# Optimization experiments

Hardware: AMD Instinct MI355X
Metric: run time of the kernel (lower is better)

## Reference

```python
import jax, jax.numpy as jnp
import numpy as np

VOCAB, EMB, HID = 32000, 128, 256
B, T = 512, 512


def setup_inputs() -> dict:
    key = jax.random.key(0)
    ks = jax.random.split(key, 6)
    x = jax.random.randint(ks[0], (B, T), 0, VOCAB, dtype=jnp.int64) if jax.config.jax_enable_x64 else jax.random.randint(ks[0], (B, T), 0, VOCAB, dtype=jnp.int32)
    s_e = 1.0 / np.sqrt(HID)
    emb = jax.random.normal(ks[1], (VOCAB, EMB), dtype=jnp.float32)
    W_ih = jax.random.uniform(ks[2], (3 * HID, EMB), dtype=jnp.float32, minval=-s_e, maxval=s_e)
    W_hh = jax.random.uniform(ks[3], (3 * HID, HID), dtype=jnp.float32, minval=-s_e, maxval=s_e)
    b_ih = jax.random.uniform(ks[4], (3 * HID,), dtype=jnp.float32, minval=-s_e, maxval=s_e)
    b_hh = jax.random.uniform(ks[5], (3 * HID,), dtype=jnp.float32, minval=-s_e, maxval=s_e)
    return {"x": x, "emb": emb, "W_ih": W_ih, "W_hh": W_hh, "b_ih": b_ih, "b_hh": b_hh}


def reference(x, emb, W_ih, W_hh, b_ih, b_hh):
    # in_len = x.shape[0] per original code (loops x[:, t, :] for t in range(x.shape[0]))
    in_len = x.shape[0]
    H = W_hh.shape[1]
    xe = emb[x]                                   # [B, T, E]
    xs = jnp.swapaxes(xe[:, :in_len, :], 0, 1)    # [in_len, B, E]
    # precompute input-side gate projections for all timesteps (one big GEMM)
    gi = jnp.einsum('tbe,ge->tbg', xs, W_ih) + b_ih   # [in_len, B, 3H]

    def step(h, gi_t):
        gh = h @ W_hh.T + b_hh                    # [B, 3H]
        i_r, i_z, i_n = gi_t[:, :H], gi_t[:, H:2*H], gi_t[:, 2*H:]
        h_r, h_z, h_n = gh[:, :H], gh[:, H:2*H], gh[:, 2*H:]
        r = jax.nn.sigmoid(i_r + h_r)
        z = jax.nn.sigmoid(i_z + h_z)
        n = jnp.tanh(i_n + r * h_n)
        h_new = (1.0 - z) * n + z * h
        return h_new, None

    h0 = jnp.zeros((x.shape[0], H), dtype=emb.dtype)  # batch = x.shape[0]
    hT, _ = jax.lax.scan(step, h0, gi)
    return hT
```

## Files before the change

kernel.cpp:

```cpp
#include <hip/hip_runtime.h>


typedef unsigned short ushort_t;
typedef __attribute__((ext_vector_type(8))) short short8;
typedef __attribute__((ext_vector_type(4))) float float4_;
typedef __attribute__((ext_vector_type(4))) unsigned short ushort4_;

#define VOCAB 32000
#define EMB 128
#define HID 256
#define G3 768
#define BB 512
#define TT 512
#define SLOT 786432
#define BLK_BYTES 24576
#define WFIXED 8781824

__device__ __forceinline__ float b2f(ushort_t u) {
  return __uint_as_float(((unsigned)u) << 16);
}
__device__ __forceinline__ ushort_t f2b(float f) {
  unsigned u = __float_as_uint(f);
  return (ushort_t)((u + 0x7FFFu + ((u >> 16) & 1u)) >> 16);
}
__device__ __forceinline__ short8 ld8(const ushort_t* p) { return *(const short8*)p; }
__device__ __forceinline__ void gld_lds16(const void* g, void* l) {
  __builtin_amdgcn_global_load_lds((const __attribute__((address_space(1))) void*)g,
                                   (__attribute__((address_space(3))) void*)l, 16, 0, 0);
}
__device__ __forceinline__ int gi_byte(int bl, int twog) {
  return ((bl * 1536) + twog) ^ ((bl & 7) << 4);
}

__global__ void cvt_bf16_k(const float* __restrict__ s, ushort_t* __restrict__ d, int n4) {
  int i = blockIdx.x * blockDim.x + threadIdx.x;
  int stride = gridDim.x * blockDim.x;
  for (; i < n4; i += stride) {
    float4_ v = ((const float4_*)s)[i];
    ushort4_ o;
    o.x = f2b(v.x); o.y = f2b(v.y); o.z = f2b(v.z); o.w = f2b(v.w);
    ((ushort4_*)d)[i] = o;
  }
}

__global__ __launch_bounds__(256) void gi_gemm(
    const int* __restrict__ x, const ushort_t* __restrict__ emb16,
    const ushort_t* __restrict__ Wih16, const float* __restrict__ bih,
    const float* __restrict__ bhh, char* __restrict__ gic, int t0) {
  __shared__ float cb[G3];
  const int tid = threadIdx.x;
  for (int i = tid; i < G3; i += 256) cb[i] = bih[i] + (i < 512 ? bhh[i] : 0.f);
  __syncthreads();
  const int lane = tid & 63, w = tid >> 6;
  const int bl = lane & 15, kg = lane >> 4;
  const int nt0 = (blockIdx.x * 4 + w) * 4;

  short8 bfr[4][4];
#pragma unroll
  for (int j = 0; j < 4; ++j) {
    int nt = nt0 + j;
    int b = (nt & 31) * 16 + bl;
    int tok = x[b * TT + t0 + (nt >> 5)];
#pragma unroll
    for (int kt = 0; kt < 4; ++kt)
      bfr[j][kt] = ld8(emb16 + (size_t)tok * EMB + kt * 32 + kg * 8);
  }

#pragma unroll 1
  for (int mt = 0; mt < 48; ++mt) {
    short8 af[4];
#pragma unroll
    for (int kt = 0; kt < 4; ++kt)
      af[kt] = ld8(Wih16 + (mt * 16 + bl) * EMB + kt * 32 + kg * 8);
    float4_ z4 = {0.f, 0.f, 0.f, 0.f};
    float4_ acc[4] = {z4, z4, z4, z4};
#pragma unroll
    for (int kt = 0; kt < 4; ++kt) {
#pragma unroll
      for (int j = 0; j < 4; ++j)
        acc[j] = __builtin_amdgcn_mfma_f32_16x16x32_bf16(af[kt], bfr[j][kt], acc[j], 0, 0, 0);
    }
    int byte8 = gi_byte(bl, 32 * mt + 8 * kg);
#pragma unroll
    for (int j = 0; j < 4; ++j) {
      int nt = nt0 + j;
      size_t base = (size_t)(nt >> 5) * SLOT + (size_t)(nt & 31) * BLK_BYTES;
      ushort4_ o;
#pragma unroll
      for (int r = 0; r < 4; ++r)
        o[r] = f2b(acc[j][r] + cb[mt * 16 + kg * 4 + r]);
      *(ushort4_*)(gic + base + byte8) = o;
    }
  }
}

__global__ __launch_bounds__(512, 2) void gru_rec(
    const ushort_t* __restrict__ Whh16, const char* __restrict__ gic,
    const float* __restrict__ bhh, float* __restrict__ out, int t0, int C) {
  __shared__ alignas(16) ushort_t h_lds[2][16 * HID];
  __shared__ alignas(16) char gi_lds[2][BLK_BYTES];
  __shared__ float bhn_lds[HID];

  const int tid = threadIdx.x, lane = tid & 63, w = tid >> 6;
  const int bl = lane & 15, kg = lane >> 4;
  const int b0 = blockIdx.x * 16;
  const char* gblk = gic + (size_t)blockIdx.x * BLK_BYTES;

  if (t0 == 0) {
    for (int i = tid; i < 16 * HID; i += 512) h_lds[0][i] = 0;
  } else {
    for (int i = tid; i < 16 * HID; i += 512) {
      int b = i >> 8, k = i & 255;
      *(ushort_t*)((char*)h_lds[0] + (((b << 9) + 2 * k) ^ ((b & 7) << 4))) =
          f2b(out[(size_t)(b0 + b) * HID + k]);
    }
  }
  for (int i = tid; i < HID; i += 512) bhn_lds[i] = bhh[512 + i];

  short8 wf[2][3][8];
#pragma unroll
  for (int i = 0; i < 2; ++i) {
#pragma unroll
    for (int q = 0; q < 3; ++q) {
      int g = (w + 8 * i + 16 * q) * 16 + bl;
#pragma unroll
      for (int kt = 0; kt < 8; ++kt)
        wf[i][q][kt] = ld8(Whh16 + (size_t)g * HID + kt * 32 + kg * 8);
    }
  }

  float hreg[2][4];
#pragma unroll
  for (int i = 0; i < 2; ++i) {
    if (t0 == 0) {
#pragma unroll
      for (int r = 0; r < 4; ++r) hreg[i][r] = 0.f;
    } else {
      float4_ v = *(const float4_*)&out[(size_t)(b0 + bl) * HID + (w + 8 * i) * 16 + kg * 4];
#pragma unroll
      for (int r = 0; r < 4; ++r) hreg[i][r] = v[r];
    }
  }

  {
    int o = (w * 3) * 1024;
#pragma unroll
    for (int ii = 0; ii < 3; ++ii)
      gld_lds16(gblk + o + ii * 1024 + lane * 16, &gi_lds[0][o + ii * 1024]);
  }
  __syncthreads();

#pragma unroll 1
  for (int t = 0; t < C; ++t) {
    const int cur = t & 1, nxt = cur ^ 1;
    if (t + 1 < C) {
      const char* src = gblk + (size_t)(t + 1) * SLOT + (w * 3) * 1024;
#pragma unroll
      for (int ii = 0; ii < 3; ++ii)
        gld_lds16(src + ii * 1024 + lane * 16, &gi_lds[nxt][(w * 3) * 1024 + ii * 1024]);
    }

    float4_ acc[2][3];
#pragma unroll
    for (int i = 0; i < 2; ++i) {
#pragma unroll
      for (int q = 0; q < 2; ++q) {
        int byte8 = gi_byte(bl, 32 * (w + 8 * i + 16 * q) + 8 * kg);
        ushort4_ v = *(const ushort4_*)(&gi_lds[cur][byte8]);
#pragma unroll
        for (int r = 0; r < 4; ++r) acc[i][q][r] = b2f(v[r]);
      }
      acc[i][2] = *(const float4_*)&bhn_lds[(w + 8 * i) * 16 + kg * 4];
    }

#pragma unroll
    for (int kt = 0; kt < 8; ++kt) {
      int byteoff = ((bl * 512) + (kt * 32 + kg * 8) * 2) ^ ((bl & 7) << 4);
      short8 bf = *(const short8*)((const char*)h_lds[cur] + byteoff);
#pragma unroll
      for (int i = 0; i < 2; ++i) {
#pragma unroll
        for (int q = 0; q < 3; ++q)
          acc[i][q] = __builtin_amdgcn_mfma_f32_16x16x32_bf16(wf[i][q][kt], bf, acc[i][q], 0, 0, 0);
      }
    }

#pragma unroll
    for (int i = 0; i < 2; ++i) {
      int byte8n = gi_byte(bl, 32 * (32 + w + 8 * i) + 8 * kg);
      ushort4_ gv = *(const ushort4_*)(&gi_lds[cur][byte8n]);
#pragma unroll
      for (int r = 0; r < 4; ++r) {
        float xr = acc[i][0][r];
        float xz = acc[i][1][r];
        float hn = acc[i][2][r];
        float rr = __builtin_amdgcn_rcpf(1.f + __expf(-xr));
        float zz = __builtin_amdgcn_rcpf(1.f + __expf(-xz));
        float y = b2f(gv[r]) + rr * hn;
        float nn = 1.f - 2.f * __builtin_amdgcn_rcpf(1.f + __expf(2.f * y));
        hreg[i][r] = (1.f - zz) * nn + zz * hreg[i][r];
      }
      int j0 = (w + 8 * i) * 16 + kg * 4;
      unsigned lo = (unsigned)f2b(hreg[i][0]) | ((unsigned)f2b(hreg[i][1]) << 16);
      unsigned hi = (unsigned)f2b(hreg[i][2]) | ((unsigned)f2b(hreg[i][3]) << 16);
      int byte0 = (bl * 512 + j0 * 2) ^ ((bl & 7) << 4);
      char* hp = (char*)h_lds[nxt];
      *(unsigned*)(hp + byte0) = lo;
      *(unsigned*)(hp + byte0 + 4) = hi;
    }
    __syncthreads();
  }

#pragma unroll
  for (int i = 0; i < 2; ++i) {
    float4_ v = {hreg[i][0], hreg[i][1], hreg[i][2], hreg[i][3]};
    *(float4_*)&out[(size_t)(b0 + bl) * HID + (w + 8 * i) * 16 + kg * 4] = v;
  }
}

extern "C" void kernel_launch(void* const* d_in, const int* in_sizes, int n_in,
                              void* d_out, int out_size, void* d_ws, size_t ws_size,
                              hipStream_t stream) {
  const int* x = (const int*)d_in[0];
  const float* emb = (const float*)d_in[1];
  const float* Wih = (const float*)d_in[2];
  const float* Whh = (const float*)d_in[3];
  const float* bih = (const float*)d_in[4];
  const float* bhh = (const float*)d_in[5];
  float* out = (float*)d_out;

  char* ws = (char*)d_ws;
  ushort_t* emb16 = (ushort_t*)ws;
  ushort_t* Wih16 = (ushort_t*)(ws + 8192000);
  ushort_t* Whh16 = (ushort_t*)(ws + 8388608);
  char* gic = ws + WFIXED;

  size_t avail = ws_size > (size_t)WFIXED ? ws_size - (size_t)WFIXED : 0;
  int C = (int)(avail / (size_t)SLOT);
  if (C > TT) C = TT;
  if (C < 1) C = 1;

  cvt_bf16_k<<<1024, 256, 0, stream>>>(emb, emb16, (VOCAB * EMB) / 4);
  cvt_bf16_k<<<96, 256, 0, stream>>>(Wih, Wih16, (G3 * EMB) / 4);
  cvt_bf16_k<<<192, 256, 0, stream>>>(Whh, Whh16, (G3 * HID) / 4);

  for (int t0 = 0; t0 < TT; t0 += C) {
    int Cc = TT - t0 < C ? TT - t0 : C;
    gi_gemm<<<2 * Cc, 256, 0, stream>>>(x, emb16, Wih16, bih, bhh, gic, t0);
    gru_rec<<<32, 512, 0, stream>>>(Whh16, gic, bhh, out, t0, Cc);
  }
}
```

Before: 1.439 ms.

## Deepen gi prefetch ring in GRU recurrence and stage gi_gemm output through LDS

The recurrent kernel now uses a 4-slot LDS ring with a prefetch distance of three steps and explicit vmcnt waits plus raw s_barrier instead of __syncthreads. The aim is to hide global-load latency for the per-step input gate projections on the serial critical path. gi_gemm is reorganised so each block handles one batch tile for two timesteps, splitting gate rows across waves and staging results in LDS for coalesced 16-byte stores. The b_hn bias moves from LDS into registers. The hand-managed waitcnt counts are fragile if the compiler emits extra vector memory ops, and the larger LDS ring may limit occupancy.

```diff
diff --git a/kernel.cpp b/kernel.cpp
--- a/kernel.cpp
+++ b/kernel.cpp
@@ -5,6 +5,7 @@
 typedef __attribute__((ext_vector_type(8))) short short8;
 typedef __attribute__((ext_vector_type(4))) float float4_;
 typedef __attribute__((ext_vector_type(4))) unsigned short ushort4_;
+typedef __attribute__((ext_vector_type(2))) unsigned int uint2_;
 
 #define VOCAB 32000
 #define EMB 128
@@ -46,50 +47,60 @@
 __global__ __launch_bounds__(256) void gi_gemm(
     const int* __restrict__ x, const ushort_t* __restrict__ emb16,
     const ushort_t* __restrict__ Wih16, const float* __restrict__ bih,
-    const float* __restrict__ bhh, char* __restrict__ gic, int t0) {
+    const float* __restrict__ bhh, char* __restrict__ gic, int t0, int C) {
   __shared__ float cb[G3];
+  __shared__ alignas(16) char img[2][BLK_BYTES];
   const int tid = threadIdx.x;
   for (int i = tid; i < G3; i += 256) cb[i] = bih[i] + (i < 512 ? bhh[i] : 0.f);
-  __syncthreads();
   const int lane = tid & 63, w = tid >> 6;
   const int bl = lane & 15, kg = lane >> 4;
-  const int nt0 = (blockIdx.x * 4 + w) * 4;
-
-  short8 bfr[4][4];
-#pragma unroll
-  for (int j = 0; j < 4; ++j) {
-    int nt = nt0 + j;
-    int b = (nt & 31) * 16 + bl;
-    int tok = x[b * TT + t0 + (nt >> 5)];
+  const int blk = blockIdx.x & 31;
+  const int tt0 = (blockIdx.x >> 5) * 2;
+  const int nj = (C - tt0) < 2 ? 1 : 2;
+
+  short8 bfr[2][4];
+#pragma unroll
+  for (int j = 0; j < 2; ++j) {
+    int tloc = tt0 + (j < nj ? j : 0);
+    int tok = x[(blk * 16 + bl) * TT + t0 + tloc];
 #pragma unroll
     for (int kt = 0; kt < 4; ++kt)
       bfr[j][kt] = ld8(emb16 + (size_t)tok * EMB + kt * 32 + kg * 8);
   }
+  __syncthreads();
 
 #pragma unroll 1
-  for (int mt = 0; mt < 48; ++mt) {
+  for (int mi = 0; mi < 12; ++mi) {
+    int mt = w * 12 + mi;
     short8 af[4];
 #pragma unroll
     for (int kt = 0; kt < 4; ++kt)
       af[kt] = ld8(Wih16 + (mt * 16 + bl) * EMB + kt * 32 + kg * 8);
     float4_ z4 = {0.f, 0.f, 0.f, 0.f};
-    float4_ acc[4] = {z4, z4, z4, z4};
-#pragma unroll
-    for (int kt = 0; kt < 4; ++kt) {
-#pragma unroll
-      for (int j = 0; j < 4; ++j)
+    float4_ acc[2] = {z4, z4};
+#pragma unroll
+    for (int kt = 0; kt < 4; ++kt)
+#pragma unroll
+      for (int j = 0; j < 2; ++j)
         acc[j] = __builtin_amdgcn_mfma_f32_16x16x32_bf16(af[kt], bfr[j][kt], acc[j], 0, 0, 0);
-    }
     int byte8 = gi_byte(bl, 32 * mt + 8 * kg);
 #pragma unroll
-    for (int j = 0; j < 4; ++j) {
-      int nt = nt0 + j;
-      size_t base = (size_t)(nt >> 5) * SLOT + (size_t)(nt & 31) * BLK_BYTES;
+    for (int j = 0; j < 2; ++j) {
       ushort4_ o;
 #pragma unroll
-      for (int r = 0; r < 4; ++r)
-        o[r] = f2b(acc[j][r] + cb[mt * 16 + kg * 4 + r]);
-      *(ushort4_*)(gic + base + byte8) = o;
+      for (int r = 0; r < 4; ++r) o[r] = f2b(acc[j][r] + cb[mt * 16 + kg * 4 + r]);
+      *(ushort4_*)(&img[j][byte8]) = o;
+    }
+  }
+  __syncthreads();
+
+#pragma unroll
+  for (int j = 0; j < 2; ++j) {
+    if (j < nj) {
+      char* dst = gic + (size_t)(tt0 + j) * SLOT + (size_t)blk * BLK_BYTES;
+#pragma unroll
+      for (int c = 0; c < 6; ++c)
+        *(float4_*)(dst + c * 4096 + tid * 16) = *(const float4_*)(&img[j][c * 4096 + tid * 16]);
     }
   }
 }
@@ -98,8 +109,7 @@
     const ushort_t* __restrict__ Whh16, const char* __restrict__ gic,
     const float* __restrict__ bhh, float* __restrict__ out, int t0, int C) {
   __shared__ alignas(16) ushort_t h_lds[2][16 * HID];
-  __shared__ alignas(16) char gi_lds[2][BLK_BYTES];
-  __shared__ float bhn_lds[HID];
+  __shared__ alignas(16) char gi_ring[4][BLK_BYTES];
 
   const int tid = threadIdx.x, lane = tid & 63, w = tid >> 6;
   const int bl = lane & 15, kg = lane >> 4;
@@ -115,11 +125,10 @@
           f2b(out[(size_t)(b0 + b) * HID + k]);
     }
   }
-  for (int i = tid; i < HID; i += 512) bhn_lds[i] = bhh[512 + i];
 
   short8 wf[2][3][8];
 #pragma unroll
-  for (int i = 0; i < 2; ++i) {
+  for (int i = 0; i < 2; ++i)
 #pragma unroll
     for (int q = 0; q < 3; ++q) {
       int g = (w + 8 * i + 16 * q) * 16 + bl;
@@ -127,11 +136,12 @@
       for (int kt = 0; kt < 8; ++kt)
         wf[i][q][kt] = ld8(Whh16 + (size_t)g * HID + kt * 32 + kg * 8);
     }
-  }
-
+
+  float4_ bhn[2];
   float hreg[2][4];
 #pragma unroll
   for (int i = 0; i < 2; ++i) {
+    bhn[i] = *(const float4_*)&bhh[512 + (w + 8 * i) * 16 + kg * 4];
     if (t0 == 0) {
 #pragma unroll
       for (int r = 0; r < 4; ++r) hreg[i][r] = 0.f;
@@ -142,22 +152,38 @@
     }
   }
 
-  {
-    int o = (w * 3) * 1024;
-#pragma unroll
-    for (int ii = 0; ii < 3; ++ii)
-      gld_lds16(gblk + o + ii * 1024 + lane * 16, &gi_lds[0][o + ii * 1024]);
-  }
-  __syncthreads();
+  asm volatile("s_waitcnt vmcnt(0) lgkmcnt(0)" ::: "memory");
+  __builtin_amdgcn_s_barrier();
+  __builtin_amdgcn_sched_barrier(0);
+
+#pragma unroll
+  for (int tau = 0; tau < 3; ++tau) {
+    if (tau < C) {
+      const char* src = gblk + (size_t)tau * SLOT + (w * 3) * 1024 + lane * 16;
+      char* dst = &gi_ring[tau][(w * 3) * 1024];
+#pragma unroll
+      for (int ii = 0; ii < 3; ++ii) gld_lds16(src + ii * 1024, dst + ii * 1024);
+    }
+  }
 
 #pragma unroll 1
   for (int t = 0; t < C; ++t) {
-    const int cur = t & 1, nxt = cur ^ 1;
-    if (t + 1 < C) {
-      const char* src = gblk + (size_t)(t + 1) * SLOT + (w * 3) * 1024;
-#pragma unroll
-      for (int ii = 0; ii < 3; ++ii)
-        gld_lds16(src + ii * 1024 + lane * 16, &gi_lds[nxt][(w * 3) * 1024 + ii * 1024]);
+    int rem = C - 1 - t;
+    if (rem >= 2)
+      asm volatile("s_waitcnt vmcnt(6) lgkmcnt(0)" ::: "memory");
+    else if (rem == 1)
+      asm volatile("s_waitcnt vmcnt(3) lgkmcnt(0)" ::: "memory");
+    else
+      asm volatile("s_waitcnt vmcnt(0) lgkmcnt(0)" ::: "memory");
+    __builtin_amdgcn_s_barrier();
+    __builtin_amdgcn_sched_barrier(0);
+
+    const int slot = t & 3, cur = t & 1, nxt = cur ^ 1;
+    if (t + 3 < C) {
+      const char* src = gblk + (size_t)(t + 3) * SLOT + (w * 3) * 1024 + lane * 16;
+      char* dst = &gi_ring[(t + 3) & 3][(w * 3) * 1024];
+#pragma unroll
+      for (int ii = 0; ii < 3; ++ii) gld_lds16(src + ii * 1024, dst + ii * 1024);
     }
 
     float4_ acc[2][3];
@@ -166,49 +192,42 @@
 #pragma unroll
       for (int q = 0; q < 2; ++q) {
         int byte8 = gi_byte(bl, 32 * (w + 8 * i + 16 * q) + 8 * kg);
-        ushort4_ v = *(const ushort4_*)(&gi_lds[cur][byte8]);
+        ushort4_ v = *(const ushort4_*)(&gi_ring[slot][byte8]);
 #pragma unroll
         for (int r = 0; r < 4; ++r) acc[i][q][r] = b2f(v[r]);
       }
-      acc[i][2] = *(const float4_*)&bhn_lds[(w + 8 * i) * 16 + kg * 4];
+      acc[i][2] = bhn[i];
     }
 
 #pragma unroll
     for (int kt = 0; kt < 8; ++kt) {
-      int byteoff = ((bl * 512) + (kt * 32 + kg * 8) * 2) ^ ((bl & 7) << 4);
+      int byteoff = ((bl * 512) + kt * 64 + kg * 16) ^ ((bl & 7) << 4);
       short8 bf = *(const short8*)((const char*)h_lds[cur] + byteoff);
 #pragma unroll
-      for (int i = 0; i < 2; ++i) {
+      for (int i = 0; i < 2; ++i)
 #pragma unroll
         for (int q = 0; q < 3; ++q)
           acc[i][q] = __builtin_amdgcn_mfma_f32_16x16x32_bf16(wf[i][q][kt], bf, acc[i][q], 0, 0, 0);
-      }
     }
 
 #pragma unroll
     for (int i = 0; i < 2; ++i) {
       int byte8n = gi_byte(bl, 32 * (32 + w + 8 * i) + 8 * kg);
-      ushort4_ gv = *(const ushort4_*)(&gi_lds[cur][byte8n]);
+      ushort4_ gv = *(const ushort4_*)(&gi_ring[slot][byte8n]);
 #pragma unroll
       for (int r = 0; r < 4; ++r) {
-        float xr = acc[i][0][r];
-        float xz = acc[i][1][r];
-        float hn = acc[i][2][r];
-        float rr = __builtin_amdgcn_rcpf(1.f + __expf(-xr));
-        float zz = __builtin_amdgcn_rcpf(1.f + __expf(-xz));
-        float y = b2f(gv[r]) + rr * hn;
+        float rr = __builtin_amdgcn_rcpf(1.f + __expf(-acc[i][0][r]));
+        float zz = __builtin_amdgcn_rcpf(1.f + __expf(-acc[i][1][r]));
+        float y = b2f(gv[r]) + rr * acc[i][2][r];
         float nn = 1.f - 2.f * __builtin_amdgcn_rcpf(1.f + __expf(2.f * y));
         hreg[i][r] = (1.f - zz) * nn + zz * hreg[i][r];
       }
-      int j0 = (w + 8 * i) * 16 + kg * 4;
-      unsigned lo = (unsigned)f2b(hreg[i][0]) | ((unsigned)f2b(hreg[i][1]) << 16);
-      unsigned hi = (unsigned)f2b(hreg[i][2]) | ((unsigned)f2b(hreg[i][3]) << 16);
-      int byte0 = (bl * 512 + j0 * 2) ^ ((bl & 7) << 4);
-      char* hp = (char*)h_lds[nxt];
-      *(unsigned*)(hp + byte0) = lo;
-      *(unsigned*)(hp + byte0 + 4) = hi;
-    }
-    __syncthreads();
+      int byte0 = (bl * 512 + ((w + 8 * i) * 16 + kg * 4) * 2) ^ ((bl & 7) << 4);
+      uint2_ hv;
+      hv.x = (unsigned)f2b(hreg[i][0]) | ((unsigned)f2b(hreg[i][1]) << 16);
+      hv.y = (unsigned)f2b(hreg[i][2]) | ((unsigned)f2b(hreg[i][3]) << 16);
+      *(uint2_*)((char*)h_lds[nxt] + byte0) = hv;
+    }
   }
 
 #pragma unroll
@@ -246,7 +265,7 @@
 
   for (int t0 = 0; t0 < TT; t0 += C) {
     int Cc = TT - t0 < C ? TT - t0 : C;
-    gi_gemm<<<2 * Cc, 256, 0, stream>>>(x, emb16, Wih16, bih, bhh, gic, t0);
+    gi_gemm<<<((Cc + 1) / 2) * 32, 256, 0, stream>>>(x, emb16, Wih16, bih, bhh, gic, t0, Cc);
     gru_rec<<<32, 512, 0, stream>>>(Whh16, gic, bhh, out, t0, Cc);
   }
 }
```

After: 1.521 ms. 1.06x slower.

## Precompute per-vocab gate table and gather it inside a single recurrent kernel

Applied to the files above, without the earlier changes.

Instead of computing input gate projections for every (t,b) token, a table of W_ih·emb+bias is computed once per vocabulary entry (32000 rows), and the recurrent kernel gathers rows by token id via direct-to-LDS loads with a 4-deep prefetch ring. The log2(e) scaling is folded into W_hh, the table and the biases so the activations can use raw exp2 instead of expf. The chunked multi-launch loop is replaced by one persistent launch, and the step loop is unrolled by four with explicit waitcnt/barrier control. This removes the large B*T gate GEMM and its workspace traffic, but adds scattered gathers of table rows on the critical path.

```diff
diff --git a/kernel.cpp b/kernel.cpp
--- a/kernel.cpp
+++ b/kernel.cpp
@@ -5,20 +5,17 @@
 typedef __attribute__((ext_vector_type(8))) short short8;
 typedef __attribute__((ext_vector_type(4))) float float4_;
 typedef __attribute__((ext_vector_type(4))) unsigned short ushort4_;
+typedef __attribute__((ext_vector_type(2))) unsigned int uint2_;
+typedef __attribute__((ext_vector_type(4))) int int4_;
 
 #define VOCAB 32000
 #define EMB 128
 #define HID 256
 #define G3 768
-#define BB 512
 #define TT 512
-#define SLOT 786432
-#define BLK_BYTES 24576
-#define WFIXED 8781824
-
-__device__ __forceinline__ float b2f(ushort_t u) {
-  return __uint_as_float(((unsigned)u) << 16);
-}
+#define L2E 1.4426950408889634f
+#define L2E2 2.8853900817779268f
+
 __device__ __forceinline__ ushort_t f2b(float f) {
   unsigned u = __float_as_uint(f);
   return (ushort_t)((u + 0x7FFFu + ((u >> 16) & 1u)) >> 16);
@@ -28,8 +25,17 @@
   __builtin_amdgcn_global_load_lds((const __attribute__((address_space(1))) void*)g,
                                    (__attribute__((address_space(3))) void*)l, 16, 0, 0);
 }
-__device__ __forceinline__ int gi_byte(int bl, int twog) {
-  return ((bl * 1536) + twog) ^ ((bl & 7) << 4);
+__device__ __forceinline__ float exp2pos(float x) {
+#if __has_builtin(__builtin_amdgcn_exp2f)
+  return __builtin_amdgcn_exp2f(x);
+#else
+  float r; asm("v_exp_f32 %0, %1" : "=v"(r) : "v"(x)); return r;
+#endif
+}
+__device__ __forceinline__ float exp2neg(float x) { return exp2pos(-x); }
+__device__ __forceinline__ unsigned pkbf(float a, float b) {
+  unsigned r; asm("v_cvt_pk_bf16_f32 %0, %1, %2" : "=v"(r) : "v"(a), "v"(b));
+  return r;
 }
 
 __global__ void cvt_bf16_k(const float* __restrict__ s, ushort_t* __restrict__ d, int n4) {
@@ -42,84 +48,97 @@
     ((ushort4_*)d)[i] = o;
   }
 }
-
-__global__ __launch_bounds__(256) void gi_gemm(
-    const int* __restrict__ x, const ushort_t* __restrict__ emb16,
-    const ushort_t* __restrict__ Wih16, const float* __restrict__ bih,
-    const float* __restrict__ bhh, char* __restrict__ gic, int t0) {
-  __shared__ float cb[G3];
+__global__ void cvt_whh_k(const float* __restrict__ s, ushort_t* __restrict__ d) {
+  int i = blockIdx.x * blockDim.x + threadIdx.x;
+  if (i >= (G3 * HID) / 4) return;
+  float sc = ((i >> 6) < 512) ? L2E : L2E2;
+  float4_ v = ((const float4_*)s)[i];
+  ushort4_ o;
+  o.x = f2b(v.x * sc); o.y = f2b(v.y * sc); o.z = f2b(v.z * sc); o.w = f2b(v.w * sc);
+  ((ushort4_*)d)[i] = o;
+}
+
+__global__ __launch_bounds__(256) void tbl_gemm(
+    const ushort_t* __restrict__ emb16, const ushort_t* __restrict__ Wih16,
+    const float* __restrict__ bih, const float* __restrict__ bhh,
+    char* __restrict__ tb_out) {
+  __shared__ float cbs[G3];
+  __shared__ alignas(16) char img[16 * 1552];
   const int tid = threadIdx.x;
-  for (int i = tid; i < G3; i += 256) cb[i] = bih[i] + (i < 512 ? bhh[i] : 0.f);
-  __syncthreads();
+  for (int i = tid; i < G3; i += 256) {
+    float sc = (i < 512) ? L2E : L2E2;
+    cbs[i] = sc * (bih[i] + (i < 512 ? bhh[i] : 0.f));
+  }
   const int lane = tid & 63, w = tid >> 6;
   const int bl = lane & 15, kg = lane >> 4;
-  const int nt0 = (blockIdx.x * 4 + w) * 4;
-
-  short8 bfr[4][4];
-#pragma unroll
-  for (int j = 0; j < 4; ++j) {
-    int nt = nt0 + j;
-    int b = (nt & 31) * 16 + bl;
-    int tok = x[b * TT + t0 + (nt >> 5)];
-#pragma unroll
-    for (int kt = 0; kt < 4; ++kt)
-      bfr[j][kt] = ld8(emb16 + (size_t)tok * EMB + kt * 32 + kg * 8);
-  }
+  const int v0 = blockIdx.x * 16;
+
+  short8 bfr[4];
+#pragma unroll
+  for (int kt = 0; kt < 4; ++kt)
+    bfr[kt] = ld8(emb16 + (size_t)(v0 + bl) * EMB + kt * 32 + kg * 8);
+  __syncthreads();
 
 #pragma unroll 1
-  for (int mt = 0; mt < 48; ++mt) {
+  for (int mi = 0; mi < 12; ++mi) {
+    int mt = w * 12 + mi;
     short8 af[4];
 #pragma unroll
     for (int kt = 0; kt < 4; ++kt)
       af[kt] = ld8(Wih16 + (mt * 16 + bl) * EMB + kt * 32 + kg * 8);
-    float4_ z4 = {0.f, 0.f, 0.f, 0.f};
-    float4_ acc[4] = {z4, z4, z4, z4};
-#pragma unroll
-    for (int kt = 0; kt < 4; ++kt) {
-#pragma unroll
-      for (int j = 0; j < 4; ++j)
-        acc[j] = __builtin_amdgcn_mfma_f32_16x16x32_bf16(af[kt], bfr[j][kt], acc[j], 0, 0, 0);
-    }
-    int byte8 = gi_byte(bl, 32 * mt + 8 * kg);
-#pragma unroll
-    for (int j = 0; j < 4; ++j) {
-      int nt = nt0 + j;
-      size_t base = (size_t)(nt >> 5) * SLOT + (size_t)(nt & 31) * BLK_BYTES;
-      ushort4_ o;
-#pragma unroll
-      for (int r = 0; r < 4; ++r)
-        o[r] = f2b(acc[j][r] + cb[mt * 16 + kg * 4 + r]);
-      *(ushort4_*)(gic + base + byte8) = o;
-    }
-  }
-}
+    float4_ acc = {0.f, 0.f, 0.f, 0.f};
+#pragma unroll
+    for (int kt = 0; kt < 4; ++kt)
+      acc = __builtin_amdgcn_mfma_f32_16x16x32_bf16(af[kt], bfr[kt], acc, 0, 0, 0);
+    float sc = (mt < 32) ? L2E : L2E2;
+    int g0 = mt * 16 + kg * 4;
+    float v0f = fmaf(sc, acc[0], cbs[g0 + 0]);
+    float v1f = fmaf(sc, acc[1], cbs[g0 + 1]);
+    float v2f = fmaf(sc, acc[2], cbs[g0 + 2]);
+    float v3f = fmaf(sc, acc[3], cbs[g0 + 3]);
+    uint2_ o;
+    o.x = pkbf(v0f, v1f);
+    o.y = pkbf(v2f, v3f);
+    *(uint2_*)(img + bl * 1552 + mt * 32 + kg * 8) = o;
+  }
+  __syncthreads();
+
+#pragma unroll
+  for (int c = 0; c < 6; ++c) {
+    int p = c * 4096 + tid * 16;
+    int q = p >> 9;
+    int row = (q * 21846) >> 16;
+    int off = p - row * 1536;
+    float4_ v = *(const float4_*)(img + row * 1552 + off);
+    *(float4_*)(tb_out + (size_t)(v0 + row) * 1536 + off) = v;
+  }
+}
+
+#define WAITV(N) asm volatile("s_waitcnt vmcnt(" #N ") lgkmcnt(0)" ::: "memory")
 
 __global__ __launch_bounds__(512, 2) void gru_rec(
-    const ushort_t* __restrict__ Whh16, const char* __restrict__ gic,
-    const float* __restrict__ bhh, float* __restrict__ out, int t0, int C) {
-  __shared__ alignas(16) ushort_t h_lds[2][16 * HID];
-  __shared__ alignas(16) char gi_lds[2][BLK_BYTES];
-  __shared__ float bhn_lds[HID];
+    const ushort_t* __restrict__ Whh16, const char* __restrict__ tbl,
+    const float* __restrict__ bhh, const int* __restrict__ x,
+    float* __restrict__ out) {
+  __shared__ alignas(16) char smem[147456];
 
   const int tid = threadIdx.x, lane = tid & 63, w = tid >> 6;
   const int bl = lane & 15, kg = lane >> 4;
   const int b0 = blockIdx.x * 16;
-  const char* gblk = gic + (size_t)blockIdx.x * BLK_BYTES;
-
-  if (t0 == 0) {
-    for (int i = tid; i < 16 * HID; i += 512) h_lds[0][i] = 0;
-  } else {
-    for (int i = tid; i < 16 * HID; i += 512) {
-      int b = i >> 8, k = i & 255;
-      *(ushort_t*)((char*)h_lds[0] + (((b << 9) + 2 * k) ^ ((b & 7) << 4))) =
-          f2b(out[(size_t)(b0 + b) * HID + k]);
-    }
-  }
-  for (int i = tid; i < HID; i += 512) bhn_lds[i] = bhh[512 + i];
+  const int s16 = (bl & 7) << 4;
+
+  {
+    const int4_* xs = (const int4_*)(x + (size_t)b0 * TT);
+    int4_* xd = (int4_*)(smem + 114688);
+#pragma unroll
+    for (int i = 0; i < 4; ++i) xd[tid + i * 512] = xs[tid + i * 512];
+    int4_ z4 = {0, 0, 0, 0};
+    *(int4_*)(smem + 98304 + tid * 16) = z4;
+  }
 
   short8 wf[2][3][8];
 #pragma unroll
-  for (int i = 0; i < 2; ++i) {
+  for (int i = 0; i < 2; ++i)
 #pragma unroll
     for (int q = 0; q < 3; ++q) {
       int g = (w + 8 * i + 16 * q) * 16 + bl;
@@ -127,89 +146,127 @@
       for (int kt = 0; kt < 8; ++kt)
         wf[i][q][kt] = ld8(Whh16 + (size_t)g * HID + kt * 32 + kg * 8);
     }
-  }
-
+
+  int h_off[8], gi_off[2][2], gn_off[2], hw_off[2];
+#pragma unroll
+  for (int kt = 0; kt < 8; ++kt)
+    h_off[kt] = 98304 + ((bl * 512 + kt * 64 + kg * 16) ^ s16);
+#pragma unroll
+  for (int i = 0; i < 2; ++i) {
+#pragma unroll
+    for (int q = 0; q < 2; ++q)
+      gi_off[i][q] = (bl * 1536 + 32 * (w + 8 * i + 16 * q) + 8 * kg) ^ s16;
+    gn_off[i] = (bl * 1536 + 32 * (32 + w + 8 * i) + 8 * kg) ^ s16;
+    hw_off[i] = 98304 + ((bl * 512 + ((w + 8 * i) * 16 + kg * 4) * 2) ^ s16);
+  }
+
+  const int s0 = (2 * w) & 7, s1 = (2 * w + 1) & 7;
+  const unsigned inv0 = (unsigned)((lane * 16) ^ (s0 << 4));
+  const unsigned inv1 = (lane < 32) ? (unsigned)((1024 + lane * 16) ^ (s0 << 4))
+                                    : (unsigned)((lane * 16 - 512) ^ (s1 << 4));
+  const unsigned inv2 = (unsigned)((512 + lane * 16) ^ (s1 << 4));
+
+  float4_ bhn[2];
   float hreg[2][4];
 #pragma unroll
   for (int i = 0; i < 2; ++i) {
-    if (t0 == 0) {
-#pragma unroll
-      for (int r = 0; r < 4; ++r) hreg[i][r] = 0.f;
-    } else {
-      float4_ v = *(const float4_*)&out[(size_t)(b0 + bl) * HID + (w + 8 * i) * 16 + kg * 4];
-#pragma unroll
-      for (int r = 0; r < 4; ++r) hreg[i][r] = v[r];
-    }
-  }
-
+    float4_ bv = *(const float4_*)&bhh[512 + (w + 8 * i) * 16 + kg * 4];
+#pragma unroll
+    for (int r = 0; r < 4; ++r) { bhn[i][r] = L2E2 * bv[r]; hreg[i][r] = 0.f; }
+  }
+
+  const int* xp = (const int*)(smem + 114688) + 2 * w * 512;
+  __syncthreads();
+
+#pragma unroll
+  for (int tau = 0; tau < 3; ++tau) {
+    int tA = xp[tau];
+    int tB = xp[tau + 512];
+    unsigned aA = (unsigned)tA * 1536u;
+    unsigned aB = (unsigned)tB * 1536u;
+    unsigned aM = (lane < 32) ? aA : aB;
+    char* d0 = smem + tau * 24576 + w * 3072;
+    gld_lds16(tbl + aA + inv0, d0);
+    gld_lds16(tbl + aM + inv1, d0 + 1024);
+    gld_lds16(tbl + aB + inv2, d0 + 2048);
+  }
+
+#define STEP(K, SL, PAR, WN, DOPF) do { \
+    WAITV(WN); \
+    __builtin_amdgcn_s_barrier(); \
+    __builtin_amdgcn_sched_barrier(0); \
+    if (DOPF) { \
+      int tA = xp[xb + (K)]; \
+      int tB = xp[xb + (K) + 512]; \
+      unsigned aA = (unsigned)tA * 1536u; \
+      unsigned aB = (unsigned)tB * 1536u; \
+      unsigned aM = (lane < 32) ? aA : aB; \
+      char* d0 = smem + (((K) + 3) & 3) * 24576 + w * 3072; \
+      gld_lds16(tbl + aA + inv0, d0); \
+      gld_lds16(tbl + aM + inv1, d0 + 1024); \
+      gld_lds16(tbl + aB + inv2, d0 + 2048); \
+    } \
+    float4_ acc[2][3]; \
+    _Pragma("unroll") for (int i = 0; i < 2; ++i) { \
+      _Pragma("unroll") for (int q = 0; q < 2; ++q) { \
+        uint2_ dg = *(const uint2_*)(smem + (SL) * 24576 + gi_off[i][q]); \
+        acc[i][q][0] = __uint_as_float(dg.x << 16); \
+        acc[i][q][1] = __uint_as_float(dg.x & 0xFFFF0000u); \
+        acc[i][q][2] = __uint_as_float(dg.y << 16); \
+        acc[i][q][3] = __uint_as_float(dg.y & 0xFFFF0000u); \
+      } \
+      acc[i][2] = bhn[i]; \
+    } \
+    _Pragma("unroll") for (int kt = 0; kt < 8; ++kt) { \
+      short8 bf = *(const short8*)(smem + h_off[kt] + (PAR) * 8192); \
+      _Pragma("unroll") for (int i = 0; i < 2; ++i) \
+        _Pragma("unroll") for (int q = 0; q < 3; ++q) \
+          acc[i][q] = __builtin_amdgcn_mfma_f32_16x16x32_bf16(wf[i][q][kt], bf, acc[i][q], 0, 0, 0); \
+    } \
+    _Pragma("unroll") for (int i = 0; i < 2; ++i) { \
+      uint2_ gd = *(const uint2_*)(smem + (SL) * 24576 + gn_off[i]); \
+      float gn0 = __uint_as_float(gd.x << 16); \
+      float gn1 = __uint_as_float(gd.x & 0xFFFF0000u); \
+      float gn2 = __uint_as_float(gd.y << 16); \
+      float gn3 = __uint_as_float(gd.y & 0xFFFF0000u); \
+      _Pragma("unroll") for (int r = 0; r < 4; ++r) { \
+        float gnr = (r == 0) ? gn0 : (r == 1) ? gn1 : (r == 2) ? gn2 : gn3; \
+        float rr = __builtin_amdgcn_rcpf(1.f + exp2neg(acc[i][0][r])); \
+        float zz = __builtin_amdgcn_rcpf(1.f + exp2neg(acc[i][1][r])); \
+        float y = fmaf(rr, acc[i][2][r], gnr); \
+        float nn = fmaf(-2.f, __builtin_amdgcn_rcpf(1.f + exp2pos(y)), 1.f); \
+        hreg[i][r] = fmaf(zz, hreg[i][r] - nn, nn); \
+      } \
+      uint2_ hv; \
+      hv.x = pkbf(hreg[i][0], hreg[i][1]); \
+      hv.y = pkbf(hreg[i][2], hreg[i][3]); \
+      *(uint2_*)(smem + hw_off[i] + ((PAR) ^ 1) * 8192) = hv; \
+    } \
+  } while (0)
+
+#pragma unroll 1
+  for (int tb = 0; tb < 504; tb += 4) {
+    const int xb = tb + 3;
+    STEP(0, 0, 0, 6, 1);
+    STEP(1, 1, 1, 6, 1);
+    STEP(2, 2, 0, 6, 1);
+    STEP(3, 3, 1, 6, 1);
+  }
   {
-    int o = (w * 3) * 1024;
-#pragma unroll
-    for (int ii = 0; ii < 3; ++ii)
-      gld_lds16(gblk + o + ii * 1024 + lane * 16, &gi_lds[0][o + ii * 1024]);
-  }
-  __syncthreads();
-
-#pragma unroll 1
-  for (int t = 0; t < C; ++t) {
-    const int cur = t & 1, nxt = cur ^ 1;
-    if (t + 1 < C) {
-      const char* src = gblk + (size_t)(t + 1) * SLOT + (w * 3) * 1024;
-#pragma unroll
-      for (int ii = 0; ii < 3; ++ii)
-        gld_lds16(src + ii * 1024 + lane * 16, &gi_lds[nxt][(w * 3) * 1024 + ii * 1024]);
-    }
-
-    float4_ acc[2][3];
-#pragma unroll
-    for (int i = 0; i < 2; ++i) {
-#pragma unroll
-      for (int q = 0; q < 2; ++q) {
-        int byte8 = gi_byte(bl, 32 * (w + 8 * i + 16 * q) + 8 * kg);
-        ushort4_ v = *(const ushort4_*)(&gi_lds[cur][byte8]);
-#pragma unroll
-        for (int r = 0; r < 4; ++r) acc[i][q][r] = b2f(v[r]);
-      }
-      acc[i][2] = *(const float4_*)&bhn_lds[(w + 8 * i) * 16 + kg * 4];
-    }
-
-#pragma unroll
-    for (int kt = 0; kt < 8; ++kt) {
-      int byteoff = ((bl * 512) + (kt * 32 + kg * 8) * 2) ^ ((bl & 7) << 4);
-      short8 bf = *(const short8*)((const char*)h_lds[cur] + byteoff);
-#pragma unroll
-      for (int i = 0; i < 2; ++i) {
-#pragma unroll
-        for (int q = 0; q < 3; ++q)
-          acc[i][q] = __builtin_amdgcn_mfma_f32_16x16x32_bf16(wf[i][q][kt], bf, acc[i][q], 0, 0, 0);
-      }
-    }
-
-#pragma unroll
-    for (int i = 0; i < 2; ++i) {
-      int byte8n = gi_byte(bl, 32 * (32 + w + 8 * i) + 8 * kg);
-      ushort4_ gv = *(const ushort4_*)(&gi_lds[cur][byte8n]);
-#pragma unroll
-      for (int r = 0; r < 4; ++r) {
-        float xr = acc[i][0][r];
-        float xz = acc[i][1][r];
-        float hn = acc[i][2][r];
-        float rr = __builtin_amdgcn_rcpf(1.f + __expf(-xr));
-        float zz = __builtin_amdgcn_rcpf(1.f + __expf(-xz));
-        float y = b2f(gv[r]) + rr * hn;
-        float nn = 1.f - 2.f * __builtin_amdgcn_rcpf(1.f + __expf(2.f * y));
-        hreg[i][r] = (1.f - zz) * nn + zz * hreg[i][r];
-      }
-      int j0 = (w + 8 * i) * 16 + kg * 4;
-      unsigned lo = (unsigned)f2b(hreg[i][0]) | ((unsigned)f2b(hreg[i][1]) << 16);
-      unsigned hi = (unsigned)f2b(hreg[i][2]) | ((unsigned)f2b(hreg[i][3]) << 16);
-      int byte0 = (bl * 512 + j0 * 2) ^ ((bl & 7) << 4);
-      char* hp = (char*)h_lds[nxt];
-      *(unsigned*)(hp + byte0) = lo;
-      *(unsigned*)(hp + byte0 + 4) = hi;
-    }
-    __syncthreads();
-  }
+    const int xb = 507;
+    STEP(0, 0, 0, 6, 1);
+    STEP(1, 1, 1, 6, 1);
+    STEP(2, 2, 0, 6, 1);
+    STEP(3, 3, 1, 6, 1);
+  }
+  {
+    const int xb = 511;
+    STEP(0, 0, 0, 6, 1);
+    STEP(1, 1, 1, 6, 0);
+    STEP(2, 2, 0, 3, 0);
+    STEP(3, 3, 1, 0, 0);
+  }
+#undef STEP
 
 #pragma unroll
   for (int i = 0; i < 2; ++i) {
@@ -233,20 +290,11 @@
   ushort_t* emb16 = (ushort_t*)ws;
   ushort_t* Wih16 = (ushort_t*)(ws + 8192000);
   ushort_t* Whh16 = (ushort_t*)(ws + 8388608);
-  char* gic = ws + WFIXED;
-
-  size_t avail = ws_size > (size_t)WFIXED ? ws_size - (size_t)WFIXED : 0;
-  int C = (int)(avail / (size_t)SLOT);
-  if (C > TT) C = TT;
-  if (C < 1) C = 1;
+  char* tbl = ws + 8781824;
 
   cvt_bf16_k<<<1024, 256, 0, stream>>>(emb, emb16, (VOCAB * EMB) / 4);
   cvt_bf16_k<<<96, 256, 0, stream>>>(Wih, Wih16, (G3 * EMB) / 4);
-  cvt_bf16_k<<<192, 256, 0, stream>>>(Whh, Whh16, (G3 * HID) / 4);
-
-  for (int t0 = 0; t0 < TT; t0 += C) {
-    int Cc = TT - t0 < C ? TT - t0 : C;
-    gi_gemm<<<2 * Cc, 256, 0, stream>>>(x, emb16, Wih16, bih, bhh, gic, t0);
-    gru_rec<<<32, 512, 0, stream>>>(Whh16, gic, bhh, out, t0, Cc);
-  }
-}
+  cvt_whh_k<<<192, 256, 0, stream>>>(Whh, Whh16);
+  tbl_gemm<<<2000, 256, 0, stream>>>(emb16, Wih16, bih, bhh, tbl);
+  gru_rec<<<32, 512, 0, stream>>>(Whh16, tbl, bhh, x, out);
+}
```

Measured after the change: 1.772 ms. +23.1%, slower.
